# Kernel tuning notes

Hardware: AMD Instinct MI355X
Metric: run time of the kernel (lower is better)

The kernel has to match this reference:

```python
import jax, jax.numpy as jnp
import numpy as np

NTOKENS = 50257
NHID = 1024
TPC = int(np.ceil(np.sqrt(NTOKENS)))          # 225 tokens per class
NCLASSES = int(np.ceil(NTOKENS / TPC))        # 224 classes
BATCH = 2048
INITRANGE = 0.1


def setup_inputs() -> dict:
    key = jax.random.key(0)
    k1, k2, k3, k4 = jax.random.split(key, 4)
    inputs = jax.random.normal(k1, (BATCH, NHID), dtype=jnp.float32)
    labels = jax.random.randint(k2, (BATCH,), 0, NTOKENS, dtype=jnp.int32)
    W_top = jax.random.uniform(k3, (NHID, NCLASSES), dtype=jnp.float32,
                               minval=-INITRANGE, maxval=INITRANGE)
    b_top = jnp.zeros((NCLASSES,), dtype=jnp.float32)
    W_bottom = jax.random.uniform(k4, (NCLASSES, NHID, TPC), dtype=jnp.float32,
                                  minval=-INITRANGE, maxval=INITRANGE)
    b_bottom = jnp.zeros((NCLASSES, TPC), dtype=jnp.float32)
    return {"inputs": inputs, "labels": labels, "W_top": W_top, "b_top": b_top,
            "W_bottom": W_bottom, "b_bottom": b_bottom}


def reference(inputs, labels, W_top, b_top, W_bottom, b_bottom):
    # Two-level hierarchical softmax: P(word) = P(class | h) * P(word | class, h)
    batch = inputs.shape[0]
    cls = labels // TPC          # [B] class index at top level
    word = labels % TPC          # [B] word index within class

    # Top level: [B, nclasses]
    top_probs = jax.nn.softmax(inputs @ W_top + b_top, axis=1)
    p_cls = top_probs[jnp.arange(batch), cls]            # [B]

    # Bottom level: gather per-example class weights then batched matvec
    Wb = W_bottom[cls]                                    # [B, nhid, tpc]
    bb = b_bottom[cls]                                    # [B, tpc]
    bottom_logits = jnp.einsum('bd,bdk->bk', inputs, Wb) + bb
    bottom_probs = jax.nn.softmax(bottom_logits, axis=1)
    p_word = bottom_probs[jnp.arange(batch), word]        # [B]

    return p_cls * p_word
```

## Files before the change

kernel.cpp:

```cpp
#include <hip/hip_runtime.h>
#include <math.h>

#define TPC 225
#define NCLS 224
#define NHID 1024
#define BATCH 2048
#define CAP 256
#define LSTRIDE 256

__global__ __launch_bounds__(256) void hs_bucket(const int* __restrict__ labels,
                                                 int* __restrict__ bucket,
                                                 int* __restrict__ cnt) {
    __shared__ int scnt[NCLS];
    const int t = threadIdx.x;
    for (int i = t; i < NCLS; i += 256) scnt[i] = 0;
    __syncthreads();
    for (int b = t; b < BATCH; b += 256) {
        int lab = labels[b];
        int c = lab / TPC;
        int pos = atomicAdd(&scnt[c], 1);
        bucket[c * CAP + pos] = b;
    }
    __syncthreads();
    for (int i = t; i < NCLS; i += 256) cnt[i] = scnt[i];
}

template <int R, int WS>
__device__ __forceinline__ void kloop(const float* __restrict__ wp,
                                      const float* const xp[R],
                                      float acc[R]) {
    constexpr int NG = NHID / 8;
    float wv[4][8];
    float4 xv[2][R][2];
#pragma unroll
    for (int r = 0; r < R; r++) acc[r] = 0.f;

#pragma unroll
    for (int b = 0; b < 4; b++)
#pragma unroll
        for (int u = 0; u < 8; u++) wv[b][u] = wp[(size_t)(b * 8 + u) * WS];
#pragma unroll
    for (int b = 0; b < 2; b++)
#pragma unroll
        for (int r = 0; r < R; r++) {
            xv[b][r][0] = *(const float4*)(xp[r] + b * 8);
            xv[b][r][1] = *(const float4*)(xp[r] + b * 8 + 4);
        }
    const float* wiss = wp + (size_t)32 * WS;
    const float* xiss[R];
#pragma unroll
    for (int r = 0; r < R; r++) xiss[r] = xp[r] + 16;

#pragma unroll 4
    for (int g = 0; g < NG - 4; ++g) {
        const int b = g & 3, xb = g & 1;
#pragma unroll
        for (int u = 0; u < 8; u++) {
            const float w_u = wv[b][u];
#pragma unroll
            for (int r = 0; r < R; r++) {
                const float xval = ((const float*)&xv[xb][r][u >> 2])[u & 3];
                acc[r] = fmaf(xval, w_u, acc[r]);
            }
        }
#pragma unroll
        for (int u = 0; u < 8; u++) wv[b][u] = wiss[(size_t)u * WS];
        wiss += 8 * WS;
#pragma unroll
        for (int r = 0; r < R; r++) {
            xv[xb][r][0] = *(const float4*)(xiss[r]);
            xv[xb][r][1] = *(const float4*)(xiss[r] + 4);
            xiss[r] += 8;
        }
    }
#pragma unroll
    for (int g = NG - 4; g < NG; ++g) {
        const int b = g & 3, xb = g & 1;
#pragma unroll
        for (int u = 0; u < 8; u++) {
            const float w_u = wv[b][u];
#pragma unroll
            for (int r = 0; r < R; r++) {
                const float xval = ((const float*)&xv[xb][r][u >> 2])[u & 3];
                acc[r] = fmaf(xval, w_u, acc[r]);
            }
        }
        if (g + 2 < NG) {
#pragma unroll
            for (int r = 0; r < R; r++) {
                xv[xb][r][0] = *(const float4*)(xiss[r]);
                xv[xb][r][1] = *(const float4*)(xiss[r] + 4);
                xiss[r] += 8;
            }
        }
    }
}

__global__ __launch_bounds__(256, 2) void hs_tlogits(const float* __restrict__ x,
                                                     const float* __restrict__ W,
                                                     float* __restrict__ tws) {
    const int t = threadIdx.x;
    const int lane = t & 63;
    const int wave = t >> 6;
    const int r0 = (blockIdx.x >> 2) * 16 + wave * 4;
    const int tile = blockIdx.x & 3;
    const int col = tile * 56 + lane;
    const int colc = (lane < 56) ? col : (NCLS - 1);

    const float* xp[4];
#pragma unroll
    for (int r = 0; r < 4; r++) xp[r] = x + (size_t)(r0 + r) * NHID;
    float acc[4];
    kloop<4, NCLS>(W + colc, xp, acc);
    if (lane < 56) {
#pragma unroll
        for (int r = 0; r < 4; r++) tws[(size_t)(r0 + r) * LSTRIDE + col] = acc[r];
    }
}

template <int R>
__device__ __forceinline__ void btile(const float* __restrict__ x,
                                      const float* __restrict__ Wcol,
                                      const int* __restrict__ bucket_c,
                                      const int base, const int col,
                                      float* __restrict__ bws) {
    int rowid[R];
    const float* xp[R];
#pragma unroll
    for (int r = 0; r < R; r++) {
        rowid[r] = __builtin_amdgcn_readfirstlane(bucket_c[base + r]);
        xp[r] = x + (size_t)rowid[r] * NHID;
    }
    float acc[R];
    kloop<R, TPC>(Wcol, xp, acc);
    if (col < TPC) {
#pragma unroll
        for (int r = 0; r < R; r++) bws[(size_t)rowid[r] * LSTRIDE + col] = acc[r];
    }
}

__global__ __launch_bounds__(256, 2) void hs_blogits(const float* __restrict__ x,
                                                     const float* __restrict__ Wb,
                                                     const int* __restrict__ bucket,
                                                     const int* __restrict__ cnt,
                                                     float* __restrict__ bws) {
    const int c = blockIdx.x >> 2;
    const int tile = blockIdx.x & 3;
    const int n = __builtin_amdgcn_readfirstlane(cnt[c]);
    if (n == 0) return;
    const int t = threadIdx.x;
    const int lane = t & 63;
    const int wave = t >> 6;
    const int col = tile * 64 + lane;
    const int colc = (col < TPC) ? col : (TPC - 1);
    const float* Wcol = Wb + (size_t)c * (NHID * TPC) + colc;
    const int* bucket_c = bucket + c * CAP;

    const int nstrips = (n + 3) >> 2;
    for (int s = wave; s < nstrips; s += 4) {
        const int base = s * 4;
        const int R = n - base < 4 ? n - base : 4;
        switch (R) {
            case 1: btile<1>(x, Wcol, bucket_c, base, col, bws); break;
            case 2: btile<2>(x, Wcol, bucket_c, base, col, bws); break;
            case 3: btile<3>(x, Wcol, bucket_c, base, col, bws); break;
            default: btile<4>(x, Wcol, bucket_c, base, col, bws); break;
        }
    }
}

__global__ __launch_bounds__(256) void hs_finish(const float* __restrict__ tws,
                                                 const float* __restrict__ bws,
                                                 const int* __restrict__ labels,
                                                 const float* __restrict__ b_top,
                                                 const float* __restrict__ b_bot,
                                                 float* __restrict__ out) {
    const int lane = threadIdx.x & 63;
    const int wave = threadIdx.x >> 6;
    const int row = blockIdx.x * 4 + wave;
    const int label = labels[row];
    const int c = label / TPC;
    const int word = label - c * TPC;

    float p[2];
#pragma unroll
    for (int lvl = 0; lvl < 2; lvl++) {
        const int NS = lvl ? TPC : NCLS;
        const int pick = lvl ? word : c;
        const float* lws = lvl ? bws : tws;
        const float* bias = lvl ? (b_bot + c * TPC) : b_top;
        float lg[4];
#pragma unroll
        for (int j = 0; j < 4; j++) {
            int k = lane + 64 * j;
            lg[j] = (k < NS) ? lws[(size_t)row * LSTRIDE + k] + bias[k] : -INFINITY;
        }
        float m = fmaxf(fmaxf(lg[0], lg[1]), fmaxf(lg[2], lg[3]));
#pragma unroll
        for (int off = 32; off > 0; off >>= 1) m = fmaxf(m, __shfl_xor(m, off, 64));
        float s = 0.f, pp = 0.f;
#pragma unroll
        for (int j = 0; j < 4; j++) {
            int k = lane + 64 * j;
            float e = (k < NS) ? __expf(lg[j] - m) : 0.f;
            s += e;
            if (k == pick) pp = e;
        }
#pragma unroll
        for (int off = 32; off > 0; off >>= 1) {
            s += __shfl_xor(s, off, 64);
            pp += __shfl_xor(pp, off, 64);
        }
        p[lvl] = pp / s;
    }
    if (lane == 0) out[row] = p[0] * p[1];
}

extern "C" void kernel_launch(void* const* d_in, const int* in_sizes, int n_in,
                              void* d_out, int out_size, void* d_ws, size_t ws_size,
                              hipStream_t stream) {
    const float* inputs   = (const float*)d_in[0];
    const int*   labels   = (const int*)d_in[1];
    const float* W_top    = (const float*)d_in[2];
    const float* b_top    = (const float*)d_in[3];
    const float* W_bottom = (const float*)d_in[4];
    const float* b_bottom = (const float*)d_in[5];
    float* out = (float*)d_out;

    int* bucket = (int*)d_ws;
    int* cnt    = bucket + NCLS * CAP;
    float* tws  = (float*)(cnt + NCLS);
    float* bws  = tws + (size_t)BATCH * LSTRIDE;

    hs_bucket<<<1, 256, 0, stream>>>(labels, bucket, cnt);
    hs_tlogits<<<(BATCH / 16) * 4, 256, 0, stream>>>(inputs, W_top, tws);
    hs_blogits<<<NCLS * 4, 256, 0, stream>>>(inputs, W_bottom, bucket, cnt, bws);
    hs_finish<<<BATCH / 4, 256, 0, stream>>>(tws, bws, labels, b_top, b_bottom, out);
}
```

Baseline: 509.5 us.

## Split-K across waves with LDS reduction for top and bottom logit kernels

Both logit GEMV kernels are restructured into 1024-thread blocks. Waves split the hidden dimension, and partial sums are combined in shared memory. Each lane now computes four columns, and the bottom kernel handles one class per block, processing its rows in groups of 16. The aim is to raise the parallelism available per class and to cut redundant weight re-reads across row strips, at the cost of larger LDS use, extra barriers, fewer blocks and heavy register pressure from the tight launch bounds.

```diff
diff --git a/kernel.cpp b/kernel.cpp
--- a/kernel.cpp
+++ b/kernel.cpp
@@ -25,146 +25,153 @@
     for (int i = t; i < NCLS; i += 256) cnt[i] = scnt[i];
 }
 
-template <int R, int WS>
-__device__ __forceinline__ void kloop(const float* __restrict__ wp,
-                                      const float* const xp[R],
-                                      float acc[R]) {
-    constexpr int NG = NHID / 8;
-    float wv[4][8];
-    float4 xv[2][R][2];
-#pragma unroll
-    for (int r = 0; r < R; r++) acc[r] = 0.f;
-
-#pragma unroll
-    for (int b = 0; b < 4; b++)
-#pragma unroll
-        for (int u = 0; u < 8; u++) wv[b][u] = wp[(size_t)(b * 8 + u) * WS];
-#pragma unroll
-    for (int b = 0; b < 2; b++)
-#pragma unroll
-        for (int r = 0; r < R; r++) {
-            xv[b][r][0] = *(const float4*)(xp[r] + b * 8);
-            xv[b][r][1] = *(const float4*)(xp[r] + b * 8 + 4);
-        }
-    const float* wiss = wp + (size_t)32 * WS;
-    const float* xiss[R];
-#pragma unroll
-    for (int r = 0; r < R; r++) xiss[r] = xp[r] + 16;
-
-#pragma unroll 4
-    for (int g = 0; g < NG - 4; ++g) {
-        const int b = g & 3, xb = g & 1;
-#pragma unroll
-        for (int u = 0; u < 8; u++) {
-            const float w_u = wv[b][u];
-#pragma unroll
-            for (int r = 0; r < R; r++) {
-                const float xval = ((const float*)&xv[xb][r][u >> 2])[u & 3];
-                acc[r] = fmaf(xval, w_u, acc[r]);
-            }
-        }
-#pragma unroll
-        for (int u = 0; u < 8; u++) wv[b][u] = wiss[(size_t)u * WS];
-        wiss += 8 * WS;
-#pragma unroll
-        for (int r = 0; r < R; r++) {
-            xv[xb][r][0] = *(const float4*)(xiss[r]);
-            xv[xb][r][1] = *(const float4*)(xiss[r] + 4);
-            xiss[r] += 8;
-        }
-    }
-#pragma unroll
-    for (int g = NG - 4; g < NG; ++g) {
-        const int b = g & 3, xb = g & 1;
-#pragma unroll
-        for (int u = 0; u < 8; u++) {
-            const float w_u = wv[b][u];
-#pragma unroll
-            for (int r = 0; r < R; r++) {
-                const float xval = ((const float*)&xv[xb][r][u >> 2])[u & 3];
-                acc[r] = fmaf(xval, w_u, acc[r]);
-            }
-        }
-        if (g + 2 < NG) {
-#pragma unroll
-            for (int r = 0; r < R; r++) {
-                xv[xb][r][0] = *(const float4*)(xiss[r]);
-                xv[xb][r][1] = *(const float4*)(xiss[r] + 4);
-                xiss[r] += 8;
-            }
-        }
-    }
-}
-
-__global__ __launch_bounds__(256, 2) void hs_tlogits(const float* __restrict__ x,
-                                                     const float* __restrict__ W,
-                                                     float* __restrict__ tws) {
+__global__ __launch_bounds__(1024, 4) void hs_tlogits(const float* __restrict__ x,
+                                                      const float* __restrict__ W,
+                                                      float* __restrict__ tws) {
+    __shared__ float red[8 * 8 * 256];
     const int t = threadIdx.x;
     const int lane = t & 63;
     const int wave = t >> 6;
-    const int r0 = (blockIdx.x >> 2) * 16 + wave * 4;
-    const int tile = blockIdx.x & 3;
-    const int col = tile * 56 + lane;
-    const int colc = (lane < 56) ? col : (NCLS - 1);
-
+    const int wr = wave & 1;
+    const int wd = wave >> 1;
+    const int r0 = blockIdx.x * 8;
+
+    const float* pj[4];
+#pragma unroll
+    for (int j = 0; j < 4; j++) {
+        int k = 64 * j + lane;
+        pj[j] = W + (size_t)wd * 128 * NCLS + (k < NCLS ? k : NCLS - 1);
+    }
     const float* xp[4];
 #pragma unroll
-    for (int r = 0; r < 4; r++) xp[r] = x + (size_t)(r0 + r) * NHID;
-    float acc[4];
-    kloop<4, NCLS>(W + colc, xp, acc);
-    if (lane < 56) {
-#pragma unroll
-        for (int r = 0; r < 4; r++) tws[(size_t)(r0 + r) * LSTRIDE + col] = acc[r];
-    }
-}
-
-template <int R>
-__device__ __forceinline__ void btile(const float* __restrict__ x,
-                                      const float* __restrict__ Wcol,
+    for (int rl = 0; rl < 4; rl++)
+        xp[rl] = x + (size_t)(r0 + wr * 4 + rl) * NHID + wd * 128;
+
+    float acc[4][4] = {};
+    for (int dq = 0; dq < 32; ++dq) {
+        float w[4][4];
+#pragma unroll
+        for (int di = 0; di < 4; di++)
+#pragma unroll
+            for (int j = 0; j < 4; j++) w[di][j] = pj[j][di * NCLS];
+#pragma unroll
+        for (int rl = 0; rl < 4; rl++) {
+            float4 xq = *(const float4*)(xp[rl] + dq * 4);
+#pragma unroll
+            for (int di = 0; di < 4; di++) {
+                float xv = ((const float*)&xq)[di];
+#pragma unroll
+                for (int j = 0; j < 4; j++)
+                    acc[rl][j] = fmaf(xv, w[di][j], acc[rl][j]);
+            }
+        }
+#pragma unroll
+        for (int j = 0; j < 4; j++) pj[j] += 4 * NCLS;
+    }
+#pragma unroll
+    for (int rl = 0; rl < 4; rl++)
+#pragma unroll
+        for (int j = 0; j < 4; j++)
+            red[(wd * 8 + wr * 4 + rl) * 256 + 64 * j + lane] = acc[rl][j];
+    __syncthreads();
+
+    const int u = t & 255;
+    for (int r = t >> 8; r < 8; r += 4) {
+        if (u < NCLS) {
+            float s = 0.f;
+#pragma unroll
+            for (int w8 = 0; w8 < 8; w8++) s += red[(w8 * 8 + r) * 256 + u];
+            tws[(size_t)(r0 + r) * LSTRIDE + u] = s;
+        }
+    }
+}
+
+template <int RW>
+__device__ __forceinline__ void bpass(const float* __restrict__ x,
+                                      const float* __restrict__ wb,
                                       const int* __restrict__ bucket_c,
-                                      const int base, const int col,
-                                      float* __restrict__ bws) {
-    int rowid[R];
-    const float* xp[R];
-#pragma unroll
-    for (int r = 0; r < R; r++) {
-        rowid[r] = __builtin_amdgcn_readfirstlane(bucket_c[base + r]);
-        xp[r] = x + (size_t)rowid[r] * NHID;
-    }
-    float acc[R];
-    kloop<R, TPC>(Wcol, xp, acc);
-    if (col < TPC) {
-#pragma unroll
-        for (int r = 0; r < R; r++) bws[(size_t)rowid[r] * LSTRIDE + col] = acc[r];
-    }
-}
-
-__global__ __launch_bounds__(256, 2) void hs_blogits(const float* __restrict__ x,
-                                                     const float* __restrict__ Wb,
-                                                     const int* __restrict__ bucket,
-                                                     const int* __restrict__ cnt,
-                                                     float* __restrict__ bws) {
-    const int c = blockIdx.x >> 2;
-    const int tile = blockIdx.x & 3;
-    const int n = __builtin_amdgcn_readfirstlane(cnt[c]);
+                                      const int base, const int n,
+                                      const int lane, const int wr, const int wd,
+                                      float* __restrict__ red) {
+    const float* xp[RW];
+#pragma unroll
+    for (int rl = 0; rl < RW; rl++) {
+        int idx = base + wr * RW + rl;
+        int row = bucket_c[idx < n ? idx : 0];
+        xp[rl] = x + (size_t)row * NHID + wd * 256;
+    }
+    const float* pj[4];
+#pragma unroll
+    for (int j = 0; j < 4; j++) {
+        int k = 64 * j + lane;
+        pj[j] = wb + (k < TPC ? k : TPC - 1);
+    }
+    float acc[RW][4] = {};
+    for (int dq = 0; dq < 64; ++dq) {
+        float w[4][4];
+#pragma unroll
+        for (int di = 0; di < 4; di++)
+#pragma unroll
+            for (int j = 0; j < 4; j++) w[di][j] = pj[j][di * TPC];
+#pragma unroll
+        for (int rl = 0; rl < RW; rl++) {
+            float4 xq = *(const float4*)(xp[rl] + dq * 4);
+#pragma unroll
+            for (int di = 0; di < 4; di++) {
+                float xv = ((const float*)&xq)[di];
+#pragma unroll
+                for (int j = 0; j < 4; j++)
+                    acc[rl][j] = fmaf(xv, w[di][j], acc[rl][j]);
+            }
+        }
+#pragma unroll
+        for (int j = 0; j < 4; j++) pj[j] += 4 * TPC;
+    }
+#pragma unroll
+    for (int rl = 0; rl < RW; rl++)
+#pragma unroll
+        for (int j = 0; j < 4; j++)
+            red[(wd * 16 + wr * RW + rl) * 256 + 64 * j + lane] = acc[rl][j];
+}
+
+__global__ __launch_bounds__(1024, 4) void hs_blogits(const float* __restrict__ x,
+                                                      const float* __restrict__ Wb,
+                                                      const int* __restrict__ bucket,
+                                                      const int* __restrict__ cnt,
+                                                      float* __restrict__ bws) {
+    __shared__ float red[4 * 16 * 256];
+    const int c = blockIdx.x;
+    const int n = cnt[c];
     if (n == 0) return;
     const int t = threadIdx.x;
     const int lane = t & 63;
     const int wave = t >> 6;
-    const int col = tile * 64 + lane;
-    const int colc = (col < TPC) ? col : (TPC - 1);
-    const float* Wcol = Wb + (size_t)c * (NHID * TPC) + colc;
+    const int wr = wave >> 2;
+    const int wd = wave & 3;
+    const float* wb = Wb + (size_t)c * (NHID * TPC) + (size_t)wd * 256 * TPC;
     const int* bucket_c = bucket + c * CAP;
 
-    const int nstrips = (n + 3) >> 2;
-    for (int s = wave; s < nstrips; s += 4) {
-        const int base = s * 4;
-        const int R = n - base < 4 ? n - base : 4;
-        switch (R) {
-            case 1: btile<1>(x, Wcol, bucket_c, base, col, bws); break;
-            case 2: btile<2>(x, Wcol, bucket_c, base, col, bws); break;
-            case 3: btile<3>(x, Wcol, bucket_c, base, col, bws); break;
-            default: btile<4>(x, Wcol, bucket_c, base, col, bws); break;
+    for (int base = 0; base < n; base += 16) {
+        int m = n - base;
+        if (m > 16) m = 16;
+        const int RW = (m + 3) >> 2;
+        if (base) __syncthreads();
+        switch (RW) {
+            case 1: bpass<1>(x, wb, bucket_c, base, n, lane, wr, wd, red); break;
+            case 2: bpass<2>(x, wb, bucket_c, base, n, lane, wr, wd, red); break;
+            case 3: bpass<3>(x, wb, bucket_c, base, n, lane, wr, wd, red); break;
+            default: bpass<4>(x, wb, bucket_c, base, n, lane, wr, wd, red); break;
+        }
+        __syncthreads();
+        const int u = t & 255;
+        for (int r = t >> 8; r < m; r += 4) {
+            if (u < TPC) {
+                float s = 0.f;
+#pragma unroll
+                for (int w4 = 0; w4 < 4; w4++) s += red[(w4 * 16 + r) * 256 + u];
+                int row = bucket_c[base + r];
+                bws[(size_t)row * LSTRIDE + u] = s;
+            }
         }
     }
 }
@@ -233,7 +240,7 @@
     float* bws  = tws + (size_t)BATCH * LSTRIDE;
 
     hs_bucket<<<1, 256, 0, stream>>>(labels, bucket, cnt);
-    hs_tlogits<<<(BATCH / 16) * 4, 256, 0, stream>>>(inputs, W_top, tws);
-    hs_blogits<<<NCLS * 4, 256, 0, stream>>>(inputs, W_bottom, bucket, cnt, bws);
+    hs_tlogits<<<256, 1024, 0, stream>>>(inputs, W_top, tws);
+    hs_blogits<<<NCLS, 1024, 0, stream>>>(inputs, W_bottom, bucket, cnt, bws);
     hs_finish<<<BATCH / 4, 256, 0, stream>>>(tws, bws, labels, b_top, b_bottom, out);
 }
```

New measurement: 446.6 us. 12.4% less time.
